# Optimization experiments

Measured on AMD Instinct MI355X. Metric: run time of the kernel, lower is better.

Reference implementation:

```python
import jax, jax.numpy as jnp
import numpy as np

D_IN = 1024
D_OUT = 1024
NUM_HEADS = 16
HEAD_DIM = D_OUT // NUM_HEADS

def setup_inputs() -> dict:
    key = jax.random.key(0)
    ks = jax.random.split(key, 6)
    b, t = 2, 2048
    s = 0.02
    return {
        "x": jax.random.normal(ks[0], (b, t, D_IN), dtype=jnp.float32),
        "Wq": jax.random.normal(ks[1], (D_IN, D_OUT), dtype=jnp.float32) * s,
        "Wk": jax.random.normal(ks[2], (D_IN, D_OUT), dtype=jnp.float32) * s,
        "Wv": jax.random.normal(ks[3], (D_IN, D_OUT), dtype=jnp.float32) * s,
        "Wo": jax.random.normal(ks[4], (D_OUT, D_OUT), dtype=jnp.float32) * s,
        "bo": jax.random.normal(ks[5], (D_OUT,), dtype=jnp.float32) * s,
    }

def reference(x, Wq, Wk, Wv, Wo, bo):
    b, t, _ = x.shape
    # QKV projections -> [b, h, t, d]
    def split_heads(y):
        return y.reshape(b, t, NUM_HEADS, HEAD_DIM).transpose(0, 2, 1, 3)
    q = split_heads(x @ Wq)
    k = split_heads(x @ Wk)
    v = split_heads(x @ Wv)
    # scores [b, h, t, t], causal mask, softmax over keys
    scores = jnp.einsum('bhqd,bhkd->bhqk', q, k)
    causal = jnp.tril(jnp.ones((t, t), dtype=bool))  # True where allowed
    scores = jnp.where(causal, scores, -jnp.inf)
    attn = jax.nn.softmax(scores / jnp.sqrt(jnp.float32(HEAD_DIM)), axis=-1)
    ctx = jnp.einsum('bhqk,bhkd->bhqd', attn, v)
    ctx = ctx.transpose(0, 2, 1, 3).reshape(b, t, D_OUT)
    return ctx @ Wo + bo
```

## Files before the change

### kernel.cpp

```cpp
#include <hip/hip_runtime.h>
#include <hip/hip_bf16.h>
#include <cstdint>
#include <cstddef>


typedef __bf16 bf16_t;
typedef __bf16 bf16x8 __attribute__((ext_vector_type(8)));
typedef float  f32x4  __attribute__((ext_vector_type(4)));

#define B_SZ 2
#define T_SZ 2048
#define DIN  1024
#define NH   16
#define HD   64

#define SCL_Q (0.125f * 1.44269504088896f)

__device__ __forceinline__ void gld_lds16(const void* g, void* l) {
    __builtin_amdgcn_global_load_lds(
        (const __attribute__((address_space(1))) void*)g,
        (__attribute__((address_space(3))) void*)l,
        16, 0, 0);
}

__global__ __launch_bounds__(256) void cvt_x_kernel(const float* __restrict__ src,
                                                    bf16_t* __restrict__ dst) {
    int i = blockIdx.x * blockDim.x + threadIdx.x;
    size_t base = (size_t)i * 8;
    float4 a = *(const float4*)(src + base);
    float4 b = *(const float4*)(src + base + 4);
    bf16x8 v;
    v[0] = (bf16_t)a.x; v[1] = (bf16_t)a.y; v[2] = (bf16_t)a.z; v[3] = (bf16_t)a.w;
    v[4] = (bf16_t)b.x; v[5] = (bf16_t)b.y; v[6] = (bf16_t)b.z; v[7] = (bf16_t)b.w;
    *(bf16x8*)(dst + base) = v;
}

__global__ __launch_bounds__(256) void transpose_cvt_kernel(const float* __restrict__ src,
                                                            bf16_t* __restrict__ dst,
                                                            int R, int C) {
    __shared__ float tile[32][33];
    int c0 = blockIdx.x * 32, r0 = blockIdx.y * 32;
    int tx = threadIdx.x, ty = threadIdx.y;
#pragma unroll
    for (int i = 0; i < 32; i += 8)
        tile[ty + i][tx] = src[(size_t)(r0 + ty + i) * C + c0 + tx];
    __syncthreads();
#pragma unroll
    for (int i = 0; i < 32; i += 8)
        dst[(size_t)(c0 + ty + i) * R + r0 + tx] = (bf16_t)tile[tx][ty + i];
}

__device__ __forceinline__ void gemm_tile_body(const bf16_t* __restrict__ A,
                                               const bf16_t* __restrict__ Bt,
                                               int m0, int n0, int K,
                                               f32x4 acc[4][4],
                                               bf16_t* As, bf16_t* Bs) {
    const int tid  = threadIdx.x;
    const int lane = tid & 63;
    const int wave = tid >> 6;
    const int wr   = (wave >> 1) * 64;
    const int wc   = (wave & 1) * 64;

#pragma unroll
    for (int mi = 0; mi < 4; ++mi)
#pragma unroll
        for (int ni = 0; ni < 4; ++ni)
            acc[mi][ni] = (f32x4){0.f, 0.f, 0.f, 0.f};

    for (int k0 = 0; k0 < K; k0 += 32) {
#pragma unroll
        for (int c = 0; c < 2; ++c) {
            int fb = (wave * 2 + c) * 1024;
            int e  = (fb >> 1) + lane * 8;
            int r  = e >> 5;
            int kk = e & 31;
            gld_lds16(A  + (size_t)(m0 + r) * K + k0 + kk, (char*)As + fb);
            gld_lds16(Bt + (size_t)(n0 + r) * K + k0 + kk, (char*)Bs + fb);
        }
        __syncthreads();

        bf16x8 af[4], bfr[4];
#pragma unroll
        for (int mi = 0; mi < 4; ++mi)
            af[mi] = *(const bf16x8*)(As + (wr + mi * 16 + (lane & 15)) * 32 + ((lane >> 4) * 8));
#pragma unroll
        for (int ni = 0; ni < 4; ++ni)
            bfr[ni] = *(const bf16x8*)(Bs + (wc + ni * 16 + (lane & 15)) * 32 + ((lane >> 4) * 8));
#pragma unroll
        for (int mi = 0; mi < 4; ++mi)
#pragma unroll
            for (int ni = 0; ni < 4; ++ni)
                acc[mi][ni] = __builtin_amdgcn_mfma_f32_16x16x32_bf16(af[mi], bfr[ni], acc[mi][ni], 0, 0, 0);
        __syncthreads();
    }
}

__global__ __launch_bounds__(256, 2) void gemm_qkv_kernel(const bf16_t* __restrict__ A,
                                                          const bf16_t* __restrict__ Bt,
                                                          bf16_t* __restrict__ Qb,
                                                          bf16_t* __restrict__ Kb,
                                                          bf16_t* __restrict__ Vt) {
    __shared__ alignas(16) bf16_t As[128 * 32];
    __shared__ alignas(16) bf16_t Bs[128 * 32];
    const int nTn = 3072 / 128;
    int m0 = (blockIdx.x / nTn) * 128;
    int n0 = (blockIdx.x % nTn) * 128;
    f32x4 acc[4][4];
    gemm_tile_body(A, Bt, m0, n0, DIN, acc, As, Bs);

    const int lane = threadIdx.x & 63;
    const int wave = threadIdx.x >> 6;
    const int wr = (wave >> 1) * 64, wc = (wave & 1) * 64;
#pragma unroll
    for (int mi = 0; mi < 4; ++mi)
#pragma unroll
        for (int ni = 0; ni < 4; ++ni)
#pragma unroll
            for (int j = 0; j < 4; ++j) {
                int m = m0 + wr + mi * 16 + ((lane >> 4) * 4) + j;
                int n = n0 + wc + ni * 16 + (lane & 15);
                int b = m >> 11, t = m & 2047;
                int part = n >> 10, c = n & 1023;
                int h = c >> 6, d = c & 63;
                float av = acc[mi][ni][j];
                if (part == 0)
                    Qb[(((size_t)(b * NH + h) * T_SZ + t) << 6) + d] = (bf16_t)(av * SCL_Q);
                else if (part == 1)
                    Kb[(((size_t)(b * NH + h) * T_SZ + t) << 6) + d] = (bf16_t)av;
                else
                    Vt[((size_t)(b * NH + h) * HD + d) * T_SZ + t] = (bf16_t)av;
            }
}

__global__ __launch_bounds__(256, 2) void attn_kernel(const bf16_t* __restrict__ Qb,
                                                      const bf16_t* __restrict__ Kb,
                                                      const bf16_t* __restrict__ Vt,
                                                      bf16_t* __restrict__ ctx) {
    __shared__ alignas(16) bf16_t Ks[2][64 * 64];
    __shared__ alignas(16) bf16_t Vs[2][64 * 64];
    __shared__ alignas(16) bf16_t P_lds[4][16][72];

    const int raw = blockIdx.x;
    const int xcd = raw & 7;
    const int jj  = raw >> 3;
    const int bh  = xcd * 4 + (jj & 3);
    const int qt  = 31 - (jj >> 2);

    const int lane = threadIdx.x & 63;
    const int wave = threadIdx.x >> 6;

    const bf16_t* Qp = Qb + (size_t)bh * T_SZ * HD;
    const bf16_t* Kp = Kb + (size_t)bh * T_SZ * HD;
    const bf16_t* Vp = Vt + (size_t)bh * HD * T_SZ;

    const int q0 = qt * 64 + wave * 16;
    const int rgrp = lane >> 4;
    const int rcol = lane & 15;

    const int st_r  = (lane >> 3);
    const int st_sl = lane & 7;

    bf16x8 qa[2];
#pragma unroll
    for (int s = 0; s < 2; ++s)
        qa[s] = *(const bf16x8*)(Qp + (size_t)(q0 + rcol) * HD + s * 32 + rgrp * 8);

    f32x4 o[4];
#pragma unroll
    for (int di = 0; di < 4; ++di) o[di] = (f32x4){0.f, 0.f, 0.f, 0.f};
    float mrun[4], lrun[4];
#pragma unroll
    for (int j = 0; j < 4; ++j) { mrun[j] = -__builtin_inff(); lrun[j] = 0.f; }

#define STAGE(BUF, KT)                                                          \
    {                                                                           \
        const int k0s = (KT) * 64;                                              \
        _Pragma("unroll")                                                       \
        for (int c = 0; c < 2; ++c) {                                           \
            int r0 = (wave * 2 + c) * 8;                                        \
            int r  = r0 + st_r;                                                 \
            int sl = st_sl ^ (r & 7);                                           \
            gld_lds16(Kp + (size_t)(k0s + r) * HD + sl * 8,                     \
                      (char*)&Ks[BUF][0] + r0 * 128);                           \
            gld_lds16(Vp + (size_t)r * T_SZ + k0s + sl * 8,                     \
                      (char*)&Vs[BUF][0] + r0 * 128);                           \
        }                                                                       \
    }

    STAGE(0, 0);
    __syncthreads();
    int buf = 0;

    for (int kt = 0; kt <= qt; ++kt) {
        if (kt < qt) STAGE(buf ^ 1, kt + 1);

        const char* Kb_l = (const char*)&Ks[buf][0];
        const char* Vb_l = (const char*)&Vs[buf][0];

        f32x4 s_acc[4];
#pragma unroll
        for (int ni = 0; ni < 4; ++ni) s_acc[ni] = (f32x4){0.f, 0.f, 0.f, 0.f};
#pragma unroll
        for (int s = 0; s < 2; ++s)
#pragma unroll
            for (int ni = 0; ni < 4; ++ni) {
                int fr = ni * 16 + rcol;
                bf16x8 kb = *(const bf16x8*)(Kb_l + fr * 128 + (((s * 4 + rgrp) ^ (fr & 7)) << 4));
                s_acc[ni] = __builtin_amdgcn_mfma_f32_16x16x32_bf16(qa[s], kb, s_acc[ni], 0, 0, 0);
            }

        float ptile[4][4];
        float mt[4];
#pragma unroll
        for (int j = 0; j < 4; ++j) mt[j] = -__builtin_inff();
        if (kt == qt) {
#pragma unroll
            for (int ni = 0; ni < 4; ++ni)
#pragma unroll
                for (int j = 0; j < 4; ++j) {
                    int q = q0 + rgrp * 4 + j;
                    int kidx = qt * 64 + ni * 16 + rcol;
                    float v = s_acc[ni][j];
                    if (kidx > q) v = -__builtin_inff();
                    ptile[ni][j] = v;
                    mt[j] = fmaxf(mt[j], v);
                }
        } else {
#pragma unroll
            for (int ni = 0; ni < 4; ++ni)
#pragma unroll
                for (int j = 0; j < 4; ++j) {
                    float v = s_acc[ni][j];
                    ptile[ni][j] = v;
                    mt[j] = fmaxf(mt[j], v);
                }
        }
#pragma unroll
        for (int j = 0; j < 4; ++j) {
            float m = mt[j];
            m = fmaxf(m, __shfl_xor(m, 1));
            m = fmaxf(m, __shfl_xor(m, 2));
            m = fmaxf(m, __shfl_xor(m, 4));
            m = fmaxf(m, __shfl_xor(m, 8));
            mt[j] = m;
        }
        bool need = false;
#pragma unroll
        for (int j = 0; j < 4; ++j) need |= (mt[j] > mrun[j] + 8.f);
        const bool full = !__all(!need);
        float alpha[4];
        if (full) {
#pragma unroll
            for (int j = 0; j < 4; ++j) {
                float newm = fmaxf(mrun[j], mt[j]);
                alpha[j] = exp2f(mrun[j] - newm);
                mrun[j] = newm;
            }
        }
        float rsum[4];
#pragma unroll
        for (int j = 0; j < 4; ++j) rsum[j] = 0.f;
#pragma unroll
        for (int ni = 0; ni < 4; ++ni)
#pragma unroll
            for (int j = 0; j < 4; ++j) {
                float p = exp2f(ptile[ni][j] - mrun[j]);
                ptile[ni][j] = p;
                rsum[j] += p;
            }
#pragma unroll
        for (int j = 0; j < 4; ++j) {
            float r = rsum[j];
            r += __shfl_xor(r, 1);
            r += __shfl_xor(r, 2);
            r += __shfl_xor(r, 4);
            r += __shfl_xor(r, 8);
            rsum[j] = r;
        }
        if (full) {
#pragma unroll
            for (int j = 0; j < 4; ++j) lrun[j] = lrun[j] * alpha[j] + rsum[j];
#pragma unroll
            for (int di = 0; di < 4; ++di)
#pragma unroll
                for (int j = 0; j < 4; ++j)
                    o[di][j] *= alpha[j];
        } else {
#pragma unroll
            for (int j = 0; j < 4; ++j) lrun[j] += rsum[j];
        }
#pragma unroll
        for (int ni = 0; ni < 4; ++ni)
#pragma unroll
            for (int j = 0; j < 4; ++j)
                P_lds[wave][rgrp * 4 + j][ni * 16 + rcol] = (bf16_t)ptile[ni][j];
#pragma unroll
        for (int s = 0; s < 2; ++s) {
            bf16x8 pa = *(const bf16x8*)(&P_lds[wave][rcol][s * 32 + rgrp * 8]);
#pragma unroll
            for (int di = 0; di < 4; ++di) {
                int fv = di * 16 + rcol;
                bf16x8 vb = *(const bf16x8*)(Vb_l + fv * 128 + (((s * 4 + rgrp) ^ (fv & 7)) << 4));
                o[di] = __builtin_amdgcn_mfma_f32_16x16x32_bf16(pa, vb, o[di], 0, 0, 0);
            }
        }
        __syncthreads();
        buf ^= 1;
    }
#undef STAGE

    const int b = bh >> 4, h = bh & 15;
    float invl[4];
#pragma unroll
    for (int j = 0; j < 4; ++j) invl[j] = 1.f / lrun[j];
#pragma unroll
    for (int di = 0; di < 4; ++di)
#pragma unroll
        for (int j = 0; j < 4; ++j) {
            int q = q0 + rgrp * 4 + j;
            int d = di * 16 + rcol;
            ctx[((size_t)(b * T_SZ + q) * NH + h) * HD + d] = (bf16_t)(o[di][j] * invl[j]);
        }
}

__global__ __launch_bounds__(256, 2) void gemm_out_kernel(const bf16_t* __restrict__ A,
                                                          const bf16_t* __restrict__ Bt,
                                                          const float* __restrict__ bias,
                                                          float* __restrict__ out) {
    __shared__ alignas(16) bf16_t As[128 * 32];
    __shared__ alignas(16) bf16_t Bs[128 * 32];
    const int nTn = 1024 / 128;
    int m0 = (blockIdx.x / nTn) * 128;
    int n0 = (blockIdx.x % nTn) * 128;
    f32x4 acc[4][4];
    gemm_tile_body(A, Bt, m0, n0, DIN, acc, As, Bs);

    const int lane = threadIdx.x & 63;
    const int wave = threadIdx.x >> 6;
    const int wr = (wave >> 1) * 64, wc = (wave & 1) * 64;
#pragma unroll
    for (int mi = 0; mi < 4; ++mi)
#pragma unroll
        for (int ni = 0; ni < 4; ++ni) {
            int n = n0 + wc + ni * 16 + (lane & 15);
            float bv = bias[n];
#pragma unroll
            for (int j = 0; j < 4; ++j) {
                int m = m0 + wr + mi * 16 + ((lane >> 4) * 4) + j;
                out[(size_t)m * 1024 + n] = acc[mi][ni][j] + bv;
            }
        }
}

extern "C" void kernel_launch(void* const* d_in, const int* in_sizes, int n_in,
                              void* d_out, int out_size, void* d_ws, size_t ws_size,
                              hipStream_t stream) {
    const float* x  = (const float*)d_in[0];
    const float* Wq = (const float*)d_in[1];
    const float* Wk = (const float*)d_in[2];
    const float* Wv = (const float*)d_in[3];
    const float* Wo = (const float*)d_in[4];
    const float* bo = (const float*)d_in[5];
    float* out = (float*)d_out;

    char* ws = (char*)d_ws;
    bf16_t* x_bf   = (bf16_t*)(ws);
    bf16_t* Wqkv_t = (bf16_t*)(ws + ((size_t)8 << 20));
    bf16_t* Wo_t   = (bf16_t*)(ws + ((size_t)14 << 20));
    bf16_t* Qb     = (bf16_t*)(ws + ((size_t)16 << 20));
    bf16_t* Kb     = (bf16_t*)(ws + ((size_t)24 << 20));
    bf16_t* Vt     = (bf16_t*)(ws + ((size_t)32 << 20));
    bf16_t* ctx    = (bf16_t*)(ws + ((size_t)40 << 20));

    cvt_x_kernel<<<2048, 256, 0, stream>>>(x, x_bf);
    transpose_cvt_kernel<<<dim3(32, 32), dim3(32, 8), 0, stream>>>(Wq, Wqkv_t, 1024, 1024);
    transpose_cvt_kernel<<<dim3(32, 32), dim3(32, 8), 0, stream>>>(Wk, Wqkv_t + (size_t)1024 * 1024, 1024, 1024);
    transpose_cvt_kernel<<<dim3(32, 32), dim3(32, 8), 0, stream>>>(Wv, Wqkv_t + (size_t)2048 * 1024, 1024, 1024);
    transpose_cvt_kernel<<<dim3(32, 32), dim3(32, 8), 0, stream>>>(Wo, Wo_t, 1024, 1024);
    gemm_qkv_kernel<<<32 * 24, 256, 0, stream>>>(x_bf, Wqkv_t, Qb, Kb, Vt);
    attn_kernel<<<B_SZ * NH * 32, 256, 0, stream>>>(Qb, Kb, Vt, ctx);
    gemm_out_kernel<<<32 * 8, 256, 0, stream>>>(ctx, Wo_t, bo, out);
}
```

Baseline: 216.9 us.

## Transpose QK^T MFMA so softmax row stats live per lane

Swaps the MFMA operands for the score tile so each lane holds one query row's scores. Row max and row sum then need only two cross-lane shuffles instead of sixteen per tile, and the running max and sum shrink to one scalar per lane. It also preloads the V fragments before the softmax, writes P to LDS as packed bf16 pairs, and raises launch bounds to three blocks per SM. The cost is extra shuffles to broadcast the rescale factors back into the output layout, plus register pressure from the V preload under the tighter occupancy target.

```diff
diff --git a/kernel.cpp b/kernel.cpp
--- a/kernel.cpp
+++ b/kernel.cpp
@@ -5,6 +5,7 @@
 
 
 typedef __bf16 bf16_t;
+typedef __bf16 bf16x2 __attribute__((ext_vector_type(2)));
 typedef __bf16 bf16x8 __attribute__((ext_vector_type(8)));
 typedef float  f32x4  __attribute__((ext_vector_type(4)));
 
@@ -132,7 +133,7 @@
             }
 }
 
-__global__ __launch_bounds__(256, 2) void attn_kernel(const bf16_t* __restrict__ Qb,
+__global__ __launch_bounds__(256, 3) void attn_kernel(const bf16_t* __restrict__ Qb,
                                                       const bf16_t* __restrict__ Kb,
                                                       const bf16_t* __restrict__ Vt,
                                                       bf16_t* __restrict__ ctx) {
@@ -168,9 +169,8 @@
     f32x4 o[4];
 #pragma unroll
     for (int di = 0; di < 4; ++di) o[di] = (f32x4){0.f, 0.f, 0.f, 0.f};
-    float mrun[4], lrun[4];
-#pragma unroll
-    for (int j = 0; j < 4; ++j) { mrun[j] = -__builtin_inff(); lrun[j] = 0.f; }
+    float mrun = -__builtin_inff();
+    float lrun = 0.f;
 
 #define STAGE(BUF, KT)                                                          \
     {                                                                           \
@@ -206,24 +206,31 @@
             for (int ni = 0; ni < 4; ++ni) {
                 int fr = ni * 16 + rcol;
                 bf16x8 kb = *(const bf16x8*)(Kb_l + fr * 128 + (((s * 4 + rgrp) ^ (fr & 7)) << 4));
-                s_acc[ni] = __builtin_amdgcn_mfma_f32_16x16x32_bf16(qa[s], kb, s_acc[ni], 0, 0, 0);
+                s_acc[ni] = __builtin_amdgcn_mfma_f32_16x16x32_bf16(kb, qa[s], s_acc[ni], 0, 0, 0);
+            }
+
+        bf16x8 vf[2][4];
+#pragma unroll
+        for (int s = 0; s < 2; ++s)
+#pragma unroll
+            for (int di = 0; di < 4; ++di) {
+                int fv = di * 16 + rcol;
+                vf[s][di] = *(const bf16x8*)(Vb_l + fv * 128 + (((s * 4 + rgrp) ^ (fv & 7)) << 4));
             }
 
         float ptile[4][4];
-        float mt[4];
-#pragma unroll
-        for (int j = 0; j < 4; ++j) mt[j] = -__builtin_inff();
+        float pmax = -__builtin_inff();
         if (kt == qt) {
+            const int qabs = q0 + rcol;
 #pragma unroll
             for (int ni = 0; ni < 4; ++ni)
 #pragma unroll
                 for (int j = 0; j < 4; ++j) {
-                    int q = q0 + rgrp * 4 + j;
-                    int kidx = qt * 64 + ni * 16 + rcol;
+                    int kidx = qt * 64 + ni * 16 + rgrp * 4 + j;
                     float v = s_acc[ni][j];
-                    if (kidx > q) v = -__builtin_inff();
+                    if (kidx > qabs) v = -__builtin_inff();
                     ptile[ni][j] = v;
-                    mt[j] = fmaxf(mt[j], v);
+                    pmax = fmaxf(pmax, v);
                 }
         } else {
 #pragma unroll
@@ -232,77 +239,57 @@
                 for (int j = 0; j < 4; ++j) {
                     float v = s_acc[ni][j];
                     ptile[ni][j] = v;
-                    mt[j] = fmaxf(mt[j], v);
+                    pmax = fmaxf(pmax, v);
                 }
         }
-#pragma unroll
-        for (int j = 0; j < 4; ++j) {
-            float m = mt[j];
-            m = fmaxf(m, __shfl_xor(m, 1));
-            m = fmaxf(m, __shfl_xor(m, 2));
-            m = fmaxf(m, __shfl_xor(m, 4));
-            m = fmaxf(m, __shfl_xor(m, 8));
-            mt[j] = m;
-        }
-        bool need = false;
-#pragma unroll
-        for (int j = 0; j < 4; ++j) need |= (mt[j] > mrun[j] + 8.f);
-        const bool full = !__all(!need);
-        float alpha[4];
-        if (full) {
+        pmax = fmaxf(pmax, __shfl_xor(pmax, 16));
+        pmax = fmaxf(pmax, __shfl_xor(pmax, 32));
+
+        const bool fullb = __any(pmax > mrun + 8.f);
+        float a_self = 1.f;
+        if (fullb) {
+            float newm = fmaxf(mrun, pmax);
+            a_self = exp2f(mrun - newm);
+            mrun = newm;
+        }
+        float rsum = 0.f;
+#pragma unroll
+        for (int ni = 0; ni < 4; ++ni)
 #pragma unroll
             for (int j = 0; j < 4; ++j) {
-                float newm = fmaxf(mrun[j], mt[j]);
-                alpha[j] = exp2f(mrun[j] - newm);
-                mrun[j] = newm;
-            }
-        }
-        float rsum[4];
-#pragma unroll
-        for (int j = 0; j < 4; ++j) rsum[j] = 0.f;
-#pragma unroll
-        for (int ni = 0; ni < 4; ++ni)
+                float p = exp2f(ptile[ni][j] - mrun);
+                ptile[ni][j] = p;
+                rsum += p;
+            }
+        rsum += __shfl_xor(rsum, 16);
+        rsum += __shfl_xor(rsum, 32);
+        if (fullb) {
+            lrun = lrun * a_self + rsum;
 #pragma unroll
             for (int j = 0; j < 4; ++j) {
-                float p = exp2f(ptile[ni][j] - mrun[j]);
-                ptile[ni][j] = p;
-                rsum[j] += p;
-            }
-#pragma unroll
-        for (int j = 0; j < 4; ++j) {
-            float r = rsum[j];
-            r += __shfl_xor(r, 1);
-            r += __shfl_xor(r, 2);
-            r += __shfl_xor(r, 4);
-            r += __shfl_xor(r, 8);
-            rsum[j] = r;
-        }
-        if (full) {
-#pragma unroll
-            for (int j = 0; j < 4; ++j) lrun[j] = lrun[j] * alpha[j] + rsum[j];
-#pragma unroll
-            for (int di = 0; di < 4; ++di)
-#pragma unroll
-                for (int j = 0; j < 4; ++j)
-                    o[di][j] *= alpha[j];
+                float aj = __shfl(a_self, (lane & 48) | (rgrp * 4 + j));
+#pragma unroll
+                for (int di = 0; di < 4; ++di) o[di][j] *= aj;
+            }
         } else {
-#pragma unroll
-            for (int j = 0; j < 4; ++j) lrun[j] += rsum[j];
-        }
-#pragma unroll
-        for (int ni = 0; ni < 4; ++ni)
-#pragma unroll
-            for (int j = 0; j < 4; ++j)
-                P_lds[wave][rgrp * 4 + j][ni * 16 + rcol] = (bf16_t)ptile[ni][j];
+            lrun += rsum;
+        }
+
+#pragma unroll
+        for (int ni = 0; ni < 4; ++ni)
+#pragma unroll
+            for (int jp = 0; jp < 2; ++jp) {
+                bf16x2 pk;
+                pk[0] = (bf16_t)ptile[ni][2 * jp];
+                pk[1] = (bf16_t)ptile[ni][2 * jp + 1];
+                *(bf16x2*)&P_lds[wave][rcol][ni * 16 + rgrp * 4 + 2 * jp] = pk;
+            }
 #pragma unroll
         for (int s = 0; s < 2; ++s) {
             bf16x8 pa = *(const bf16x8*)(&P_lds[wave][rcol][s * 32 + rgrp * 8]);
 #pragma unroll
-            for (int di = 0; di < 4; ++di) {
-                int fv = di * 16 + rcol;
-                bf16x8 vb = *(const bf16x8*)(Vb_l + fv * 128 + (((s * 4 + rgrp) ^ (fv & 7)) << 4));
-                o[di] = __builtin_amdgcn_mfma_f32_16x16x32_bf16(pa, vb, o[di], 0, 0, 0);
-            }
+            for (int di = 0; di < 4; ++di)
+                o[di] = __builtin_amdgcn_mfma_f32_16x16x32_bf16(pa, vf[s][di], o[di], 0, 0, 0);
         }
         __syncthreads();
         buf ^= 1;
@@ -312,7 +299,10 @@
     const int b = bh >> 4, h = bh & 15;
     float invl[4];
 #pragma unroll
-    for (int j = 0; j < 4; ++j) invl[j] = 1.f / lrun[j];
+    for (int j = 0; j < 4; ++j) {
+        float lj = __shfl(lrun, (lane & 48) | (rgrp * 4 + j));
+        invl[j] = 1.f / lj;
+    }
 #pragma unroll
     for (int di = 0; di < 4; ++di)
 #pragma unroll
```

New measurement: 194.7 us. -10.2%, faster.
